# Kernel optimization log

Measured on AMD Instinct MI355X. Metric: run time of the kernel, lower is better.

Reference implementation:

```python
import jax, jax.numpy as jnp
import numpy as np

N_QUBITS = 10      # = hidden_dim; state vector has 2**10 = 1024 amplitudes
T, B, D = 128, 256, 64
H = N_QUBITS
DIM = 2 ** N_QUBITS


def _rx(theta):
    # RX(t) = [[cos(t/2), -i sin(t/2)], [-i sin(t/2), cos(t/2)]]; theta scalar or (B,)
    c = jnp.cos(theta / 2).astype(jnp.complex64)
    s = (-1j) * jnp.sin(theta / 2).astype(jnp.complex64)
    return jnp.stack([jnp.stack([c, s], -1), jnp.stack([s, c], -1)], -2)


def _ry(theta):
    c = jnp.cos(theta / 2)
    s = jnp.sin(theta / 2)
    return jnp.stack([jnp.stack([c, -s], -1), jnp.stack([s, c], -1)], -2).astype(jnp.complex64)


def _rz(theta):
    em = jnp.exp(-0.5j * theta.astype(jnp.complex64))
    ep = jnp.exp(0.5j * theta.astype(jnp.complex64))
    z = jnp.zeros_like(em)
    return jnp.stack([jnp.stack([em, z], -1), jnp.stack([z, ep], -1)], -2)


def _apply_1q(state, mat, w):
    # state: (B, 2^n) complex; wire 0 is the most-significant axis (torchquantum layout)
    b = state.shape[0]
    s = state.reshape(b, 2 ** w, 2, -1)
    if mat.ndim == 2:
        out = jnp.einsum('ij,bljr->blir', mat, s)
    else:  # batched encoding angles: mat (B,2,2)
        out = jnp.einsum('bij,bljr->blir', mat, s)
    return out.reshape(b, -1)


def _apply_cnot(state, a, bq):
    # control a < target bq: flip target axis in the control=1 block
    b = state.shape[0]
    s = state.reshape(b, 2 ** a, 2, 2 ** (bq - a - 1), 2, -1)
    new = jnp.stack([s[:, :, 0], s[:, :, 1, :, ::-1]], axis=2)
    return new.reshape(b, -1)


def qgate(x, params):
    # x: (B, n) classical features -> PauliZ expectations per wire (B, n)
    n = N_QUBITS
    b = x.shape[0]
    state = jnp.zeros((b, 2 ** n), jnp.complex64).at[:, 0].set(1.0 + 0.0j)
    for w in range(n):                       # RX encoding of input features
        state = _apply_1q(state, _rx(x[:, w]), w)
    for w in range(n):                       # parameterized RX, RY, RZ per wire
        state = _apply_1q(state, _rx(params[w, 0]), w)
        state = _apply_1q(state, _ry(params[w, 1]), w)
        state = _apply_1q(state, _rz(params[w, 2]), w)
    for a in range(n - 1):                   # CNOT chain entanglement
        state = _apply_cnot(state, a, a + 1)
    probs = jnp.real(state * jnp.conj(state))
    zs = []
    for w in range(n):                       # <Z_w> = P(bit_w=0) - P(bit_w=1)
        p = probs.reshape(b, 2 ** w, 2, -1)
        zs.append(p[:, :, 0, :].sum((1, 2)) - p[:, :, 1, :].sum((1, 2)))
    return jnp.stack(zs, axis=1)


def setup_inputs() -> dict:
    key = jax.random.key(0)
    ks = jax.random.split(key, 16)
    scale = 1.0 / np.sqrt(D + H)
    inp = {'inputs': jax.random.normal(ks[0], (T, B, D), jnp.float32)}
    for i, g in enumerate(['f', 'i', 'u', 'o']):
        inp['W' + g] = jax.random.normal(ks[1 + 3 * i], (H, D + H), jnp.float32) * scale
        inp['b' + g] = jax.random.normal(ks[2 + 3 * i], (H,), jnp.float32) * scale
        inp['p' + g] = jax.random.normal(ks[3 + 3 * i], (H, 3), jnp.float32)
    inp['ln_g'] = jnp.ones((H,), jnp.float32)
    inp['ln_b'] = jnp.zeros((H,), jnp.float32)
    return inp


def reference(inputs, Wf, bf, pf, Wi, bi, pi, Wu, bu, pu, Wo, bo, po, ln_g, ln_b):
    b = inputs.shape[1]

    def step(carry, x):
        hx, cx = carry
        comb = jnp.concatenate([x, hx], axis=1)
        f = jax.nn.sigmoid(qgate(comb @ Wf.T + bf, pf))
        i = jax.nn.sigmoid(qgate(comb @ Wi.T + bi, pi))
        g = jnp.tanh(qgate(comb @ Wu.T + bu, pu))
        o = jax.nn.sigmoid(qgate(comb @ Wo.T + bo, po))
        cx2 = f * cx + i * g
        h = o * jnp.tanh(cx2) + hx  # residual skip
        mu = h.mean(-1, keepdims=True)
        var = ((h - mu) ** 2).mean(-1, keepdims=True)
        h = (h - mu) / jnp.sqrt(var + 1e-5) * ln_g + ln_b  # LayerNorm
        # dropout: identity in eval mode
        return (h, cx2), h

    init = (jnp.zeros((b, H), jnp.float32), jnp.zeros((b, H), jnp.float32))
    (hx, cx), ys = jax.lax.scan(step, init, inputs)
    return ys, hx, cx
```

## Files before the change

kernel.cpp:

```cpp
#include <hip/hip_runtime.h>
#include <math.h>


#define T_STEPS 128
#define B_SZ    256
#define D_IN    64
#define H_SZ    10
#define COMB    74
#define ZPAD    132

#define INV2PI  0.15915494f

__device__ __forceinline__ float rdlane(float v, int lane) {
    return __int_as_float(__builtin_amdgcn_readlane(__float_as_int(v), lane));
}
__device__ __forceinline__ float frcp(float x) { return __builtin_amdgcn_rcpf(x); }

__device__ __forceinline__ float tanh_pade(float x) {
    float x2  = x * x;
    float num = x * fmaf(x2, (x2 + 105.f), 945.f);
    float den = fmaf(x2, fmaf(x2, 15.f, 420.f), 945.f);
    return num * frcp(den);
}

__global__ __launch_bounds__(128) void qlstm_fused(
    const float* __restrict__ x,
    const float* __restrict__ Wf, const float* __restrict__ bf, const float* __restrict__ pf,
    const float* __restrict__ Wi, const float* __restrict__ bi, const float* __restrict__ pi,
    const float* __restrict__ Wu, const float* __restrict__ bu, const float* __restrict__ pu,
    const float* __restrict__ Wo, const float* __restrict__ bo, const float* __restrict__ po,
    const float* __restrict__ ln_g, const float* __restrict__ ln_b,
    float* __restrict__ ys, float* __restrict__ outH, float* __restrict__ outC)
{
    __shared__ __align__(16) float Wl[40 * 64];
    __shared__ __align__(16) float Zl[40 * ZPAD];
    __shared__ __align__(16) float ys_l[T_STEPS * H_SZ + 64];
    __shared__ float bl[40];
    __shared__ float p0l[40];

    const int tid = threadIdx.x;
    const int b   = blockIdx.x;

    float xr[64];
    const float4* xin = (const float4*)(x + ((size_t)tid * B_SZ + b) * D_IN);
#pragma unroll
    for (int k = 0; k < 16; k++) {
        float4 v = xin[k];
        xr[4*k+0] = v.x; xr[4*k+1] = v.y; xr[4*k+2] = v.z; xr[4*k+3] = v.w;
    }

#pragma unroll
    for (int k = 0; k < 20; k++) {
        int idx = k * 128 + tid;
        int r   = idx >> 6;
        int col = idx & 63;
        const float* Wp; int w;
        if      (r < 10) { Wp = Wf; w = r;      }
        else if (r < 20) { Wp = Wi; w = r - 10; }
        else if (r < 30) { Wp = Wu; w = r - 20; }
        else             { Wp = Wo; w = r - 30; }
        Wl[idx] = Wp[w * COMB + col];
    }
    if (tid < 40) {
        int r = tid;
        const float* bp; const float* pp; int w;
        if      (r < 10) { bp = bf; pp = pf; w = r;      }
        else if (r < 20) { bp = bi; pp = pi; w = r - 10; }
        else if (r < 30) { bp = bu; pp = pu; w = r - 20; }
        else             { bp = bo; pp = po; w = r - 30; }
        bl[tid]  = bp[w];
        p0l[tid] = pp[w * 3];
    }
    __syncthreads();

#pragma unroll
    for (int gw = 0; gw < 40; gw++) {
        float a = bl[gw];
        const float4* wr4 = (const float4*)(Wl + gw * 64);
#pragma unroll
        for (int d4 = 0; d4 < 16; d4++) {
            float4 wv = wr4[d4];
            a = fmaf(xr[4*d4+0], wv.x, a);
            a = fmaf(xr[4*d4+1], wv.y, a);
            a = fmaf(xr[4*d4+2], wv.z, a);
            a = fmaf(xr[4*d4+3], wv.w, a);
        }
        Zl[gw * ZPAD + tid] = (a + p0l[gw]) * INV2PI;
    }
    __syncthreads();

    if (tid >= 64) return;

    const int lane = tid;
    const int g    = lane >> 4;
    const int w    = lane & 15;
    const bool act = (w < H_SZ);

    const float* Ws[4] = {Wf, Wi, Wu, Wo};
    const float* ps[4] = {pf, pi, pu, po};

    float whp[H_SZ];
    float S = 0.f, A = 0.f;
#pragma unroll
    for (int j = 0; j < H_SZ; j++) {
        float whj = act ? Ws[g][w * COMB + D_IN + j] : 0.f;
        whp[j] = whj * ln_g[j] * INV2PI;
        S += whp[j];
        A  = fmaf(whj, ln_b[j], A);
    }
    A *= INV2PI;

    const float cp1 = act ? __cosf(ps[g][w * 3 + 1]) : 1.f;
    const float lng = act ? ln_g[w] : 0.f;
    const float lnb = act ? ln_b[w] : 0.f;
    const float s1 = (g == 2) ? 1.f : 0.5f;
    const float sc = (g == 2) ? 1.f : 0.5f;
    const float s0l = (act ? ((g == 2) ? 0.f : 0.5f) : 0.f);

    float cpp = cp1;
    asm("s_nop 1\n\t"
        "v_mul_f32_dpp %0, %0, %0 row_shr:1 row_mask:0xf bank_mask:0xf\n\t"
        "s_nop 1\n\t"
        "v_mul_f32_dpp %0, %0, %0 row_shr:2 row_mask:0xf bank_mask:0xf\n\t"
        "s_nop 1\n\t"
        "v_mul_f32_dpp %0, %0, %0 row_shr:4 row_mask:0xf bank_mask:0xf\n\t"
        "s_nop 1\n\t"
        "v_mul_f32_dpp %0, %0, %0 row_shr:8 row_mask:0xf bank_mask:0xf"
        : "+v"(cpp));

    const float TAc = 0.999904f, TBc = -0.331065f,
                TCc = 0.120472f, TDc = -0.027717f;
    const float kk  = sc * cpp;
    const float k2  = kk * kk;
    const float qa  = act ? s1 * TAc * kk            : 0.f;
    const float qb  = act ? s1 * TBc * kk * k2       : 0.f;
    const float qc  = act ? s1 * TCc * kk * k2 * k2  : 0.f;
    const float qd  = act ? s1 * TDc * kk * k2 * k2 * k2 : 0.f;

    float hn = 0.f;
    float cc = 0.f;
    float htr = 0.f;

    const int gwl = g * 10 + (act ? w : 9);
    const float* zb = Zl + (size_t)gwl * ZPAD;
    float4 zb0 = *(const float4*)(zb);
    float4 zb1 = *(const float4*)(zb + 4);

    float* ysl = ys_l + lane;

    for (int gq = 0; gq < T_STEPS / 4; gq++) {
        float4 zc = zb0;
        zb0 = zb1;
        const int nl = (gq + 2 < T_STEPS / 4) ? gq + 2 : T_STEPS / 4 - 1;
        zb1 = *(const float4*)(zb + (size_t)nl * 4);

        float zs[4] = {zc.x, zc.y, zc.z, zc.w};
#pragma unroll
        for (int j = 0; j < 4; j++) {
            const int t = gq * 4 + j;

            float r = zs[j] + htr;
            float cv;
            asm("v_fract_f32 %0, %1\n\t"
                "v_cos_f32 %0, %0\n\t"
                "s_nop 1"
                : "=v"(cv) : "v"(r));

            float prod = cv;
            asm("s_nop 1\n\t"
                "v_mul_f32_dpp %0, %0, %0 row_shr:1 row_mask:0xf bank_mask:0xf\n\t"
                "s_nop 1\n\t"
                "v_mul_f32_dpp %0, %0, %0 row_shr:2 row_mask:0xf bank_mask:0xf\n\t"
                "s_nop 1\n\t"
                "v_mul_f32_dpp %0, %0, %0 row_shr:4 row_mask:0xf bank_mask:0xf\n\t"
                "s_nop 1\n\t"
                "v_mul_f32_dpp %0, %0, %0 row_shr:8 row_mask:0xf bank_mask:0xf"
                : "+v"(prod));

            float y  = prod * prod;
            float qp = fmaf(y, qd, qc);
            qp       = fmaf(y, qp, qb);
            qp       = fmaf(y, qp, qa);
            float av = fmaf(prod, qp, s0l);

            float a_ = av, b_ = av;
            asm("s_nop 1\n\t"
                "v_permlane32_swap_b32 %0, %1" : "+v"(a_), "+v"(b_));
            float F_ = a_, I_ = a_;
            asm("s_nop 1\n\t"
                "v_permlane16_swap_b32 %0, %1" : "+v"(F_), "+v"(I_));
            float U_ = b_, O_ = b_;
            asm("s_nop 1\n\t"
                "v_permlane16_swap_b32 %0, %1" : "+v"(U_), "+v"(O_));

            cc = fmaf(F_, cc, I_ * U_);
            float tc   = tanh_pade(cc);
            float hraw = fmaf(O_, tc, hn);

            float v1 = hraw * 0.1f;
            float v2 = v1 * hraw;
            asm("s_nop 1\n\t"
                "v_add_f32_dpp %0, %0, %0 row_ror:8 row_mask:0xf bank_mask:0xf\n\t"
                "v_add_f32_dpp %1, %1, %1 row_ror:8 row_mask:0xf bank_mask:0xf\n\t"
                "s_nop 0\n\t"
                "v_add_f32_dpp %0, %0, %0 row_ror:4 row_mask:0xf bank_mask:0xf\n\t"
                "v_add_f32_dpp %1, %1, %1 row_ror:4 row_mask:0xf bank_mask:0xf\n\t"
                "s_nop 0\n\t"
                "v_add_f32_dpp %0, %0, %0 row_ror:2 row_mask:0xf bank_mask:0xf\n\t"
                "v_add_f32_dpp %1, %1, %1 row_ror:2 row_mask:0xf bank_mask:0xf\n\t"
                "s_nop 0\n\t"
                "v_add_f32_dpp %0, %0, %0 row_ror:1 row_mask:0xf bank_mask:0xf\n\t"
                "v_add_f32_dpp %1, %1, %1 row_ror:1 row_mask:0xf bank_mask:0xf"
                : "+v"(v1), "+v"(v2));

            float d0 = whp[0] * rdlane(hraw, 0);
            float d1 = whp[1] * rdlane(hraw, 1);
            d0 = fmaf(whp[2], rdlane(hraw, 2), d0);
            d1 = fmaf(whp[3], rdlane(hraw, 3), d1);
            d0 = fmaf(whp[4], rdlane(hraw, 4), d0);
            d1 = fmaf(whp[5], rdlane(hraw, 5), d1);
            d0 = fmaf(whp[6], rdlane(hraw, 6), d0);
            d1 = fmaf(whp[7], rdlane(hraw, 7), d1);
            d0 = fmaf(whp[8], rdlane(hraw, 8), d0);
            d1 = fmaf(whp[9], rdlane(hraw, 9), d1);
            float D = d0 + d1;

            float mu   = v1;
            float rstd = __builtin_amdgcn_rsqf(v2 + fmaf(-mu, mu, 1e-5f));
            float hc   = hraw - mu;

            hn  = fmaf(hc * rstd, lng, lnb);
            htr = fmaf(rstd, fmaf(-mu, S, D), A);

            ysl[t * H_SZ] = hn;
        }
    }

#pragma unroll
    for (int k = 0; k < 20; k++) {
        int idx = k * 64 + lane;
        int t   = idx / H_SZ;
        int ww  = idx - t * H_SZ;
        ys[(size_t)t * B_SZ * H_SZ + (size_t)b * H_SZ + ww] = ys_l[idx];
    }

    if (lane < H_SZ) {
        outH[b * H_SZ + lane] = hn;
        outC[b * H_SZ + lane] = cc;
    }
}

extern "C" void kernel_launch(void* const* d_in, const int* in_sizes, int n_in,
                              void* d_out, int out_size, void* d_ws, size_t ws_size,
                              hipStream_t stream)
{
    const float* x    = (const float*)d_in[0];
    const float* Wf   = (const float*)d_in[1];
    const float* bf   = (const float*)d_in[2];
    const float* pf   = (const float*)d_in[3];
    const float* Wi   = (const float*)d_in[4];
    const float* bi   = (const float*)d_in[5];
    const float* pi   = (const float*)d_in[6];
    const float* Wu   = (const float*)d_in[7];
    const float* bu   = (const float*)d_in[8];
    const float* pu   = (const float*)d_in[9];
    const float* Wo   = (const float*)d_in[10];
    const float* bo   = (const float*)d_in[11];
    const float* po   = (const float*)d_in[12];
    const float* ln_g = (const float*)d_in[13];
    const float* ln_b = (const float*)d_in[14];

    float* ys   = (float*)d_out;
    float* outH = ys + (size_t)T_STEPS * B_SZ * H_SZ;
    float* outC = outH + (size_t)B_SZ * H_SZ;

    qlstm_fused<<<B_SZ, 128, 0, stream>>>(
        x, Wf, bf, pf, Wi, bi, pi, Wu, bu, pu, Wo, bo, po,
        ln_g, ln_b, ys, outH, outC);
}
```

Measured before the change: 124.3 us.

## Spread input projection over 1024 threads and shorten recurrent dependency chain

The block grows from 128 to 1024 threads, and each group of 128 computes only 5 of the 40 gate-row projections for all timesteps instead of one thread doing all 40. This cuts the serial precompute time per block. In the recurrent loop, the polynomial is evaluated Estrin-style and the tanh reciprocal is folded into the output-gate product, which shortens the per-step latency chain. Each thread still loads the full 64-float x row, so x reads repeat eight times, and the larger block may affect register allocation and occupancy.

```diff
diff --git a/kernel.cpp b/kernel.cpp
--- a/kernel.cpp
+++ b/kernel.cpp
@@ -16,14 +16,7 @@
 }
 __device__ __forceinline__ float frcp(float x) { return __builtin_amdgcn_rcpf(x); }
 
-__device__ __forceinline__ float tanh_pade(float x) {
-    float x2  = x * x;
-    float num = x * fmaf(x2, (x2 + 105.f), 945.f);
-    float den = fmaf(x2, fmaf(x2, 15.f, 420.f), 945.f);
-    return num * frcp(den);
-}
-
-__global__ __launch_bounds__(128) void qlstm_fused(
+__global__ __launch_bounds__(1024) void qlstm_fused(
     const float* __restrict__ x,
     const float* __restrict__ Wf, const float* __restrict__ bf, const float* __restrict__ pf,
     const float* __restrict__ Wi, const float* __restrict__ bi, const float* __restrict__ pi,
@@ -39,10 +32,12 @@
     __shared__ float p0l[40];
 
     const int tid = threadIdx.x;
+    const int grp = tid >> 7;
+    const int tt  = tid & 127;
     const int b   = blockIdx.x;
 
     float xr[64];
-    const float4* xin = (const float4*)(x + ((size_t)tid * B_SZ + b) * D_IN);
+    const float4* xin = (const float4*)(x + ((size_t)tt * B_SZ + b) * D_IN);
 #pragma unroll
     for (int k = 0; k < 16; k++) {
         float4 v = xin[k];
@@ -50,16 +45,18 @@
     }
 
 #pragma unroll
-    for (int k = 0; k < 20; k++) {
-        int idx = k * 128 + tid;
-        int r   = idx >> 6;
-        int col = idx & 63;
-        const float* Wp; int w;
-        if      (r < 10) { Wp = Wf; w = r;      }
-        else if (r < 20) { Wp = Wi; w = r - 10; }
-        else if (r < 30) { Wp = Wu; w = r - 20; }
-        else             { Wp = Wo; w = r - 30; }
-        Wl[idx] = Wp[w * COMB + col];
+    for (int k = 0; k < 3; k++) {
+        int idx = k * 1024 + tid;
+        if (idx < 2560) {
+            int r   = idx >> 6;
+            int col = idx & 63;
+            const float* Wp; int w;
+            if      (r < 10) { Wp = Wf; w = r;      }
+            else if (r < 20) { Wp = Wi; w = r - 10; }
+            else if (r < 30) { Wp = Wu; w = r - 20; }
+            else             { Wp = Wo; w = r - 30; }
+            Wl[idx] = Wp[w * COMB + col];
+        }
     }
     if (tid < 40) {
         int r = tid;
@@ -74,7 +71,8 @@
     __syncthreads();
 
 #pragma unroll
-    for (int gw = 0; gw < 40; gw++) {
+    for (int i = 0; i < 5; i++) {
+        const int gw = grp * 5 + i;
         float a = bl[gw];
         const float4* wr4 = (const float4*)(Wl + gw * 64);
 #pragma unroll
@@ -85,7 +83,7 @@
             a = fmaf(xr[4*d4+2], wv.z, a);
             a = fmaf(xr[4*d4+3], wv.w, a);
         }
-        Zl[gw * ZPAD + tid] = (a + p0l[gw]) * INV2PI;
+        Zl[gw * ZPAD + tt] = (a + p0l[gw]) * INV2PI;
     }
     __syncthreads();
 
@@ -178,9 +176,10 @@
                 : "+v"(prod));
 
             float y  = prod * prod;
-            float qp = fmaf(y, qd, qc);
-            qp       = fmaf(y, qp, qb);
-            qp       = fmaf(y, qp, qa);
+            float t0 = fmaf(y, qb, qa);
+            float t1 = fmaf(y, qd, qc);
+            float y2 = y * y;
+            float qp = fmaf(y2, t1, t0);
             float av = fmaf(prod, qp, s0l);
 
             float a_ = av, b_ = av;
@@ -194,11 +193,16 @@
                 "v_permlane16_swap_b32 %0, %1" : "+v"(U_), "+v"(O_));
 
             cc = fmaf(F_, cc, I_ * U_);
-            float tc   = tanh_pade(cc);
-            float hraw = fmaf(O_, tc, hn);
+
+            float x2  = cc * cc;
+            float num = cc * fmaf(x2, (x2 + 105.f), 945.f);
+            float den = fmaf(x2, fmaf(x2, 15.f, 420.f), 945.f);
+            float rd  = frcp(den);
+            float on  = O_ * num;
+            float hraw = fmaf(on, rd, hn);
 
             float v1 = hraw * 0.1f;
-            float v2 = v1 * hraw;
+            float v2 = hraw * hraw;
             asm("s_nop 1\n\t"
                 "v_add_f32_dpp %0, %0, %0 row_ror:8 row_mask:0xf bank_mask:0xf\n\t"
                 "v_add_f32_dpp %1, %1, %1 row_ror:8 row_mask:0xf bank_mask:0xf\n\t"
@@ -226,7 +230,8 @@
             float D = d0 + d1;
 
             float mu   = v1;
-            float rstd = __builtin_amdgcn_rsqf(v2 + fmaf(-mu, mu, 1e-5f));
+            float rstd = __builtin_amdgcn_rsqf(
+                             fmaf(v2, 0.1f, fmaf(-mu, mu, 1e-5f)));
             float hc   = hraw - mu;
 
             hn  = fmaf(hc * rstd, lng, lnb);
@@ -274,7 +279,7 @@
     float* outH = ys + (size_t)T_STEPS * B_SZ * H_SZ;
     float* outC = outH + (size_t)B_SZ * H_SZ;
 
-    qlstm_fused<<<B_SZ, 128, 0, stream>>>(
+    qlstm_fused<<<B_SZ, 1024, 0, stream>>>(
         x, Wf, bf, pf, Wi, bi, pi, Wu, bu, pu, Wo, bo, po,
         ln_g, ln_b, ys, outH, outC);
 }
```

Result: faster. 120.3 us (-3.3%).
